# Performance work log

Measured on AMD Instinct MI355X. Metric: run time of the kernel, lower is better.

Reference implementation:

```python
import jax, jax.numpy as jnp
import numpy as np

N = 30000        # nodes
E = 480000       # edges (before self-loops)
F_IN = 512       # input feature dim
HID = 64         # per-head hidden dim
HEADS = 4
WIDTH = HID * HEADS  # 256, concat heads
LAYERS = 3
NCLS = 40
NEG_SLOPE = 0.2


def setup_inputs() -> dict:
    key = jax.random.key(0)
    ks = jax.random.split(key, 16)
    def p(k, shape, scale=0.1):
        return jax.random.normal(k, shape, dtype=jnp.float32) * scale
    return {
        "x": jax.random.normal(ks[0], (N, F_IN), dtype=jnp.float32),
        "edge_index": jax.random.randint(ks[1], (2, E), 0, N, dtype=jnp.int32),
        # layer 1: F_IN -> HEADS*HID (concat)
        "W1": p(ks[2], (F_IN, WIDTH)), "as1": p(ks[3], (HEADS, HID)), "ad1": p(ks[4], (HEADS, HID)), "b1": p(ks[5], (WIDTH,)),
        # layer 2: WIDTH -> WIDTH
        "W2": p(ks[6], (WIDTH, WIDTH)), "as2": p(ks[7], (HEADS, HID)), "ad2": p(ks[8], (HEADS, HID)), "b2": p(ks[9], (WIDTH,)),
        # layer 3: WIDTH -> WIDTH
        "W3": p(ks[10], (WIDTH, WIDTH)), "as3": p(ks[11], (HEADS, HID)), "ad3": p(ks[12], (HEADS, HID)), "b3": p(ks[13], (WIDTH,)),
        # JK='cat' output head: WIDTH*LAYERS -> NCLS
        "Wo": p(ks[14], (WIDTH * LAYERS, NCLS)), "bo": p(ks[15], (NCLS,)),
    }


def gat_layer(x, Wm, a_src, a_dst, b, src, dst):
    # PyG GATConv (concat=True, eval mode): h = xW reshaped [N,H,C];
    # e_ij = leaky_relu(a_src.h_j + a_dst.h_i) for edge j->i, softmax over dst groups.
    n = x.shape[0]
    H, C = a_src.shape
    h = (x @ Wm).reshape(n, H, C)                      # [N,H,C]
    es = jnp.sum(h * a_src, axis=-1)                   # [N,H]
    ed = jnp.sum(h * a_dst, axis=-1)                   # [N,H]
    e = jax.nn.leaky_relu(es[src] + ed[dst], NEG_SLOPE)  # [Etot,H]
    m = jax.ops.segment_max(e, dst, num_segments=n)    # stable softmax per dst node
    w = jnp.exp(e - m[dst])
    den = jax.ops.segment_sum(w, dst, num_segments=n)
    alpha = w / den[dst]                               # [Etot,H]
    out = jax.ops.segment_sum(h[src] * alpha[:, :, None], dst, num_segments=n)  # [N,H,C]
    return out.reshape(n, H * C) + b


def reference(x, edge_index, W1, as1, ad1, b1, W2, as2, ad2, b2, W3, as3, ad3, b3, Wo, bo):
    # add self-loops (PyG GATConv default)
    loops = jnp.arange(N, dtype=edge_index.dtype)
    src = jnp.concatenate([edge_index[0], loops])
    dst = jnp.concatenate([edge_index[1], loops])
    # dropout is identity in eval mode
    h1 = jax.nn.relu(gat_layer(x, W1, as1, ad1, b1, src, dst))
    h2 = jax.nn.relu(gat_layer(h1, W2, as2, ad2, b2, src, dst))
    h3 = jax.nn.relu(gat_layer(h2, W3, as3, ad3, b3, src, dst))
    h = jnp.concatenate([h1, h2, h3], axis=-1)         # JK 'cat': [N, WIDTH*LAYERS]
    return h @ Wo + bo                                 # [N, NCLS]
```

## Files before the change

### kernel.cpp

```cpp
#include <hip/hip_runtime.h>

#define N_NODES 30000
#define N_EDGES 480000
#define ETOT    510000
#define F_IN    512
#define WIDTH   256
#define NCLS    40
#define KCAT    768
#define NPAD    48

typedef __attribute__((ext_vector_type(8))) short short8;
typedef __attribute__((ext_vector_type(4))) float f32x4;

__device__ __forceinline__ unsigned short f2bf(float f){
  unsigned u = __float_as_uint(f);
  u += 0x7fffu + ((u >> 16) & 1u);
  return (unsigned short)(u >> 16);
}
__device__ __forceinline__ float b2f(unsigned short s){
  return __uint_as_float(((unsigned)s) << 16);
}

__global__ void transpose_w_kernel(const float* __restrict__ W, unsigned short* __restrict__ Wt,
                                   int K, int Nc){
  int k = blockIdx.x * blockDim.x + threadIdx.x;
  int n = blockIdx.y;
  if (k < K) Wt[(size_t)n * K + k] = f2bf(W[(size_t)k * Nc + n]);
}

__global__ void transpose_wo_kernel(const float* __restrict__ Wo, unsigned short* __restrict__ WoT){
  int i = blockIdx.x * blockDim.x + threadIdx.x;
  if (i < NPAD * KCAT){
    int c = i / KCAT, k = i - c * KCAT;
    WoT[i] = (c < NCLS) ? f2bf(Wo[(size_t)k * NCLS + c]) : (unsigned short)0;
  }
}

__global__ void zero_kernel(int* __restrict__ p, int n){
  int i = blockIdx.x * blockDim.x + threadIdx.x;
  if (i < n) p[i] = 0;
}

__global__ void hist_kernel(const int* __restrict__ ei, int* __restrict__ counts){
  int e = blockIdx.x * blockDim.x + threadIdx.x;
  if (e < ETOT){
    int d = (e < N_EDGES) ? ei[N_EDGES + e] : (e - N_EDGES);
    atomicAdd(&counts[d], 1);
  }
}

__global__ __launch_bounds__(1024) void scan_kernel(const int* __restrict__ counts,
                                                    int* __restrict__ offsets,
                                                    int* __restrict__ cursor, int n){
  __shared__ int wsum[16];
  int tid = threadIdx.x, lane = tid & 63, wid = tid >> 6;
  int running = 0;
  int nchunks = (n + 1023) >> 10;
  for (int ch = 0; ch < nchunks; ++ch){
    int i = (ch << 10) + tid;
    int v = (i < n) ? counts[i] : 0;
    int x = v;
    #pragma unroll
    for (int off = 1; off < 64; off <<= 1){
      int t = __shfl_up(x, off, 64);
      if (lane >= off) x += t;
    }
    if (lane == 63) wsum[wid] = x;
    __syncthreads();
    if (wid == 0){
      int s = (lane < 16) ? wsum[lane] : 0;
      #pragma unroll
      for (int off = 1; off < 16; off <<= 1){
        int t = __shfl_up(s, off, 64);
        if (lane >= off) s += t;
      }
      if (lane < 16) wsum[lane] = s;
    }
    __syncthreads();
    int waveprefix = (wid > 0) ? wsum[wid - 1] : 0;
    int excl = x - v + waveprefix + running;
    if (i < n){ offsets[i] = excl; cursor[i] = excl; }
    running += wsum[15];
    __syncthreads();
  }
  if (tid == 0) offsets[n] = running;
}

__global__ void scatter_kernel(const int* __restrict__ ei, int* __restrict__ cursor,
                               int* __restrict__ srcs){
  int e = blockIdx.x * blockDim.x + threadIdx.x;
  if (e < ETOT){
    int s, d;
    if (e < N_EDGES){ s = ei[e]; d = ei[N_EDGES + e]; }
    else { s = e - N_EDGES; d = s; }
    int pos = atomicAdd(&cursor[d], 1);
    srcs[pos] = s;
  }
}

template<int K, bool AF32>
__global__ __launch_bounds__(256) void gemm_direct_kernel(const void* __restrict__ Araw,
                                                          const unsigned short* __restrict__ Bt,
                                                          const float* __restrict__ a_s,
                                                          const float* __restrict__ a_d,
                                                          float* __restrict__ es,
                                                          float* __restrict__ ed,
                                                          unsigned short* __restrict__ hb,
                                                          int M){
  int tid = threadIdx.x, lane = tid & 63, wid = tid >> 6;
  int l15 = lane & 15, quad = lane >> 4;
  int g = wid;
  int m0 = blockIdx.x * 64;

  int arow[4];
  #pragma unroll
  for (int rt = 0; rt < 4; ++rt){
    int r = m0 + rt * 16 + l15;
    arow[rt] = (r < M) ? r : (M - 1);
  }
  const unsigned short* brow[4];
  #pragma unroll
  for (int ct = 0; ct < 4; ++ct)
    brow[ct] = Bt + (size_t)(64 * g + ct * 16 + l15) * K + quad * 8;

  f32x4 acc[4][4];
  #pragma unroll
  for (int rt = 0; rt < 4; ++rt)
    #pragma unroll
    for (int ct = 0; ct < 4; ++ct) acc[rt][ct] = (f32x4){0.f, 0.f, 0.f, 0.f};

  auto load_a = [&](int rt, int k0) -> short8 {
    if (AF32){
      const float* p = (const float*)Araw + (size_t)arow[rt] * K + k0 + quad * 8;
      float4 v0 = *(const float4*)(p);
      float4 v1 = *(const float4*)(p + 4);
      union { short8 s; ushort4 u[2]; } r;
      r.u[0] = (ushort4){f2bf(v0.x), f2bf(v0.y), f2bf(v0.z), f2bf(v0.w)};
      r.u[1] = (ushort4){f2bf(v1.x), f2bf(v1.y), f2bf(v1.z), f2bf(v1.w)};
      return r.s;
    } else {
      return *(const short8*)((const unsigned short*)Araw + (size_t)arow[rt] * K + k0 + quad * 8);
    }
  };

  short8 a_cur[4], b_cur[4], a_nxt[4], b_nxt[4];
  #pragma unroll
  for (int rt = 0; rt < 4; ++rt) a_cur[rt] = load_a(rt, 0);
  #pragma unroll
  for (int ct = 0; ct < 4; ++ct) b_cur[ct] = *(const short8*)(brow[ct]);

  for (int k0 = 0; k0 < K; k0 += 32){
    if (k0 + 32 < K){
      #pragma unroll
      for (int rt = 0; rt < 4; ++rt) a_nxt[rt] = load_a(rt, k0 + 32);
      #pragma unroll
      for (int ct = 0; ct < 4; ++ct) b_nxt[ct] = *(const short8*)(brow[ct] + k0 + 32);
    }
    #pragma unroll
    for (int rt = 0; rt < 4; ++rt)
      #pragma unroll
      for (int ct = 0; ct < 4; ++ct)
        acc[rt][ct] = __builtin_amdgcn_mfma_f32_16x16x32_bf16(a_cur[rt], b_cur[ct], acc[rt][ct], 0, 0, 0);
    #pragma unroll
    for (int rt = 0; rt < 4; ++rt) a_cur[rt] = a_nxt[rt];
    #pragma unroll
    for (int ct = 0; ct < 4; ++ct) b_cur[ct] = b_nxt[ct];
  }

  #pragma unroll
  for (int rt = 0; rt < 4; ++rt){
    int row0 = m0 + rt * 16 + quad * 4;
    #pragma unroll
    for (int i = 0; i < 4; ++i){
      int grow = row0 + i;
      unsigned vo[4];
      #pragma unroll
      for (int ct = 0; ct < 4; ++ct){
        unsigned lo = (unsigned)f2bf(acc[rt][ct][i]);
        unsigned hi = (unsigned)__shfl_xor((int)lo, 1, 64);
        vo[ct] = lo | (hi << 16);
      }
      if ((l15 & 1) == 0 && grow < M){
        unsigned short* hrow = hb + (size_t)grow * WIDTH + 64 * g + l15;
        *(unsigned*)(hrow)      = vo[0];
        *(unsigned*)(hrow + 16) = vo[1];
        *(unsigned*)(hrow + 32) = vo[2];
        *(unsigned*)(hrow + 48) = vo[3];
      }
    }
  }

  float asv[4], adv[4];
  #pragma unroll
  for (int ct = 0; ct < 4; ++ct){
    asv[ct] = a_s[g * 64 + ct * 16 + l15];
    adv[ct] = a_d[g * 64 + ct * 16 + l15];
  }
  #pragma unroll
  for (int rt = 0; rt < 4; ++rt){
    int row0 = m0 + rt * 16 + quad * 4;
    #pragma unroll
    for (int i = 0; i < 4; ++i){
      float se = acc[rt][0][i] * asv[0] + acc[rt][1][i] * asv[1]
               + acc[rt][2][i] * asv[2] + acc[rt][3][i] * asv[3];
      float sd = acc[rt][0][i] * adv[0] + acc[rt][1][i] * adv[1]
               + acc[rt][2][i] * adv[2] + acc[rt][3][i] * adv[3];
      #pragma unroll
      for (int off = 1; off < 16; off <<= 1){
        se += __shfl_xor(se, off, 64);
        sd += __shfl_xor(sd, off, 64);
      }
      int grow = row0 + i;
      if (l15 == 0 && grow < M){
        es[grow * 4 + g] = se;
        ed[grow * 4 + g] = sd;
      }
    }
  }
}

__global__ __launch_bounds__(256) void agg_kernel(const int* __restrict__ offsets,
                                                  const int* __restrict__ srcs,
                                                  const float* __restrict__ es,
                                                  const float* __restrict__ ed,
                                                  const unsigned short* __restrict__ hb,
                                                  const float* __restrict__ bias,
                                                  unsigned short* __restrict__ hout){
  __shared__ float eLds[8][64][4];
  __shared__ int   sLds[8][64];
  int wid = threadIdx.x >> 6;
  int lane = threadIdx.x & 63;
  int half = lane >> 5, l32 = lane & 31;
  int slot = wid * 2 + half;
  int n = blockIdx.x * 8 + slot;
  int base = offsets[n];
  int deg = offsets[n + 1] - base;
  float4 edv = *(const float4*)(ed + n * 4);

  float m0 = -1e30f, m1 = -1e30f, m2 = -1e30f, m3 = -1e30f;
  for (int i = l32; i < deg; i += 32){
    int s = srcs[base + i];
    float4 ev = *(const float4*)(es + s * 4);
    float e0 = ev.x + edv.x, e1 = ev.y + edv.y, e2 = ev.z + edv.z, e3 = ev.w + edv.w;
    e0 = e0 > 0.f ? e0 : 0.2f * e0;
    e1 = e1 > 0.f ? e1 : 0.2f * e1;
    e2 = e2 > 0.f ? e2 : 0.2f * e2;
    e3 = e3 > 0.f ? e3 : 0.2f * e3;
    if (i < 64){
      sLds[slot][i] = s;
      *(float4*)(&eLds[slot][i][0]) = (float4){e0, e1, e2, e3};
    }
    m0 = fmaxf(m0, e0); m1 = fmaxf(m1, e1); m2 = fmaxf(m2, e2); m3 = fmaxf(m3, e3);
  }
  #pragma unroll
  for (int off = 1; off < 32; off <<= 1){
    m0 = fmaxf(m0, __shfl_xor(m0, off, 64));
    m1 = fmaxf(m1, __shfl_xor(m1, off, 64));
    m2 = fmaxf(m2, __shfl_xor(m2, off, 64));
    m3 = fmaxf(m3, __shfl_xor(m3, off, 64));
  }
  int head = l32 >> 3;
  float mh  = (head == 0) ? m0 : (head == 1) ? m1 : (head == 2) ? m2 : m3;
  float edh = (head == 0) ? edv.x : (head == 1) ? edv.y : (head == 2) ? edv.z : edv.w;

  float2 a0 = {0.f,0.f}, a1 = {0.f,0.f}, a2 = {0.f,0.f}, a3 = {0.f,0.f};
  float den = 0.f;
  const unsigned short* hcol = hb + 8 * l32;
  for (int i = 0; i < deg; i += 8){
    int sidx[8]; float w[8];
    #pragma unroll
    for (int u = 0; u < 8; ++u){
      int idx = i + u;
      bool v = idx < deg;
      float le; int s;
      if (idx < 64 || !v){
        int ic = v ? idx : 0;
        if (ic >= 64) ic = 0;
        s  = sLds[slot][ic];
        le = eLds[slot][ic][head];
      } else {
        s = srcs[base + idx];
        float e = es[s * 4 + head] + edh;
        le = e > 0.f ? e : 0.2f * e;
      }
      sidx[u] = s;
      w[u] = v ? __expf(le - mh) : 0.f;
    }
    uint4 hv[8];
    #pragma unroll
    for (int u = 0; u < 8; ++u)
      hv[u] = *(const uint4*)(hcol + (size_t)sidx[u] * WIDTH);
    #pragma unroll
    for (int u = 0; u < 8; ++u){
      float wu = w[u];
      den += wu;
      a0.x += wu * __uint_as_float(hv[u].x << 16);
      a0.y += wu * __uint_as_float(hv[u].x & 0xffff0000u);
      a1.x += wu * __uint_as_float(hv[u].y << 16);
      a1.y += wu * __uint_as_float(hv[u].y & 0xffff0000u);
      a2.x += wu * __uint_as_float(hv[u].z << 16);
      a2.y += wu * __uint_as_float(hv[u].z & 0xffff0000u);
      a3.x += wu * __uint_as_float(hv[u].w << 16);
      a3.y += wu * __uint_as_float(hv[u].w & 0xffff0000u);
    }
  }
  float inv = 1.0f / den;
  const float* bp = bias + 8 * l32;
  float4 bv0 = *(const float4*)(bp);
  float4 bv1 = *(const float4*)(bp + 4);
  float o0 = fmaxf(a0.x * inv + bv0.x, 0.f);
  float o1 = fmaxf(a0.y * inv + bv0.y, 0.f);
  float o2 = fmaxf(a1.x * inv + bv0.z, 0.f);
  float o3 = fmaxf(a1.y * inv + bv0.w, 0.f);
  float o4 = fmaxf(a2.x * inv + bv1.x, 0.f);
  float o5 = fmaxf(a2.y * inv + bv1.y, 0.f);
  float o6 = fmaxf(a3.x * inv + bv1.z, 0.f);
  float o7 = fmaxf(a3.y * inv + bv1.w, 0.f);
  uint4 o;
  o.x = (unsigned)f2bf(o0) | ((unsigned)f2bf(o1) << 16);
  o.y = (unsigned)f2bf(o2) | ((unsigned)f2bf(o3) << 16);
  o.z = (unsigned)f2bf(o4) | ((unsigned)f2bf(o5) << 16);
  o.w = (unsigned)f2bf(o6) | ((unsigned)f2bf(o7) << 16);
  *(uint4*)(hout + (size_t)n * WIDTH + 8 * l32) = o;
}

__global__ __launch_bounds__(256) void out_gemm_kernel(const unsigned short* __restrict__ h1,
                                                       const unsigned short* __restrict__ h2,
                                                       const unsigned short* __restrict__ h3,
                                                       const unsigned short* __restrict__ WoT,
                                                       const float* __restrict__ bo,
                                                       float* __restrict__ out){
  int tid = threadIdx.x, lane = tid & 63, wid = tid >> 6;
  int l15 = lane & 15, quad = lane >> 4;
  int m0 = blockIdx.x * 64 + 16 * wid;

  f32x4 acc[3];
  #pragma unroll
  for (int t = 0; t < 3; ++t) acc[t] = (f32x4){0.f, 0.f, 0.f, 0.f};

  int arow = m0 + l15; if (arow >= N_NODES) arow = N_NODES - 1;

  #pragma unroll
  for (int part = 0; part < 3; ++part){
    const unsigned short* hp = (part == 0) ? h1 : (part == 1) ? h2 : h3;
    const unsigned short* ap = hp + (size_t)arow * WIDTH;
    #pragma unroll
    for (int k0 = 0; k0 < WIDTH; k0 += 32){
      short8 af = *(const short8*)(ap + k0 + quad * 8);
      int kk = part * WIDTH + k0;
      #pragma unroll
      for (int t = 0; t < 3; ++t){
        short8 bf = *(const short8*)(WoT + (size_t)(16 * t + l15) * KCAT + kk + quad * 8);
        acc[t] = __builtin_amdgcn_mfma_f32_16x16x32_bf16(af, bf, acc[t], 0, 0, 0);
      }
    }
  }

  int r0 = m0 + quad * 4;
  #pragma unroll
  for (int t = 0; t < 3; ++t){
    int col = 16 * t + l15;
    if (col < NCLS){
      float bc = bo[col];
      #pragma unroll
      for (int r = 0; r < 4; ++r){
        int grow = r0 + r;
        if (grow < N_NODES) out[(size_t)grow * NCLS + col] = acc[t][r] + bc;
      }
    }
  }
}

static inline size_t align256(size_t x){ return (x + 255) & ~(size_t)255; }

extern "C" void kernel_launch(void* const* d_in, const int* in_sizes, int n_in,
                              void* d_out, int out_size, void* d_ws, size_t ws_size,
                              hipStream_t stream) {
  const float* x   = (const float*)d_in[0];
  const int*   ei  = (const int*)  d_in[1];
  const float* W1  = (const float*)d_in[2];
  const float* as1 = (const float*)d_in[3];
  const float* ad1 = (const float*)d_in[4];
  const float* b1  = (const float*)d_in[5];
  const float* W2  = (const float*)d_in[6];
  const float* as2 = (const float*)d_in[7];
  const float* ad2 = (const float*)d_in[8];
  const float* b2  = (const float*)d_in[9];
  const float* W3  = (const float*)d_in[10];
  const float* as3 = (const float*)d_in[11];
  const float* ad3 = (const float*)d_in[12];
  const float* b3  = (const float*)d_in[13];
  const float* Wo  = (const float*)d_in[14];
  const float* bo  = (const float*)d_in[15];
  float* out = (float*)d_out;

  char* p = (char*)d_ws;
  auto take = [&](size_t bytes) -> char* { char* cur = p; p += align256(bytes); return cur; };

  unsigned short* Wt1   = (unsigned short*)take((size_t)WIDTH * F_IN * 2);
  unsigned short* Wt2   = (unsigned short*)take((size_t)WIDTH * WIDTH * 2);
  unsigned short* Wt3   = (unsigned short*)take((size_t)WIDTH * WIDTH * 2);
  unsigned short* WoT   = (unsigned short*)take((size_t)NPAD * KCAT * 2);
  unsigned short* hstage= (unsigned short*)take((size_t)N_NODES * WIDTH * 2);
  float*          es    = (float*)take((size_t)N_NODES * 4 * 4);
  float*          ed    = (float*)take((size_t)N_NODES * 4 * 4);
  unsigned short* h1b   = (unsigned short*)take((size_t)N_NODES * WIDTH * 2);
  unsigned short* h2b   = (unsigned short*)take((size_t)N_NODES * WIDTH * 2);
  unsigned short* h3b   = (unsigned short*)take((size_t)N_NODES * WIDTH * 2);
  int*            counts  = (int*)take((size_t)N_NODES * 4);
  int*            offsets = (int*)take((size_t)(N_NODES + 1) * 4);
  int*            cursor  = (int*)take((size_t)N_NODES * 4);
  int*            srcs    = (int*)take((size_t)ETOT * 4);

  transpose_w_kernel<<<dim3(F_IN / 256, WIDTH), 256, 0, stream>>>(W1, Wt1, F_IN, WIDTH);
  transpose_w_kernel<<<dim3(1, WIDTH), 256, 0, stream>>>(W2, Wt2, WIDTH, WIDTH);
  transpose_w_kernel<<<dim3(1, WIDTH), 256, 0, stream>>>(W3, Wt3, WIDTH, WIDTH);
  transpose_wo_kernel<<<(NPAD * KCAT + 255) / 256, 256, 0, stream>>>(Wo, WoT);

  zero_kernel<<<(N_NODES + 255) / 256, 256, 0, stream>>>(counts, N_NODES);
  hist_kernel<<<(ETOT + 255) / 256, 256, 0, stream>>>(ei, counts);
  scan_kernel<<<1, 1024, 0, stream>>>(counts, offsets, cursor, N_NODES);
  scatter_kernel<<<(ETOT + 255) / 256, 256, 0, stream>>>(ei, cursor, srcs);

  const int ntiles   = (N_NODES + 63) / 64;
  const int agg_grid = N_NODES / 8;

  gemm_direct_kernel<F_IN, true><<<ntiles, 256, 0, stream>>>(x, Wt1, as1, ad1, es, ed, hstage, N_NODES);
  agg_kernel<<<agg_grid, 256, 0, stream>>>(offsets, srcs, es, ed, hstage, b1, h1b);
  gemm_direct_kernel<WIDTH, false><<<ntiles, 256, 0, stream>>>(h1b, Wt2, as2, ad2, es, ed, hstage, N_NODES);
  agg_kernel<<<agg_grid, 256, 0, stream>>>(offsets, srcs, es, ed, hstage, b2, h2b);
  gemm_direct_kernel<WIDTH, false><<<ntiles, 256, 0, stream>>>(h2b, Wt3, as3, ad3, es, ed, hstage, N_NODES);
  agg_kernel<<<agg_grid, 256, 0, stream>>>(offsets, srcs, es, ed, hstage, b3, h3b);

  out_gemm_kernel<<<ntiles, 256, 0, stream>>>(h1b, h2b, h3b, WoT, bo, out);
}
```

Baseline: 435.9 us.

## Stage GEMM operands in LDS via global_load_lds and pre-cast x to bf16

Replaces the register-direct GEMM, where each wave loaded its own A and B fragments from global memory, with a kernel that stages a 64x32 A tile and a 256x32 B tile in LDS using async global-to-LDS loads. All four waves then share them. A separate cast kernel converts x to bf16 up front, so the first-layer GEMM reads half the bytes and does no conversion inline. The trade-off is an extra full pass over x plus a 30 MB workspace buffer. The new loop also has two barriers per K step and no software prefetch or double buffering, so load latency is no longer hidden.

```diff
diff --git a/kernel.cpp b/kernel.cpp
--- a/kernel.cpp
+++ b/kernel.cpp
@@ -19,6 +19,25 @@
 }
 __device__ __forceinline__ float b2f(unsigned short s){
   return __uint_as_float(((unsigned)s) << 16);
+}
+
+__device__ __forceinline__ void load_lds16(const void* g, void* l){
+  __builtin_amdgcn_global_load_lds((const __attribute__((address_space(1))) void*)g,
+                                   (__attribute__((address_space(3))) void*)l, 16, 0, 0);
+}
+
+__global__ void cast8_kernel(const float* __restrict__ in, unsigned short* __restrict__ out, int n8){
+  int i = blockIdx.x * blockDim.x + threadIdx.x;
+  if (i < n8){
+    const float4* p = (const float4*)(in + 8 * (size_t)i);
+    float4 v0 = p[0], v1 = p[1];
+    uint4 o;
+    o.x = (unsigned)f2bf(v0.x) | ((unsigned)f2bf(v0.y) << 16);
+    o.y = (unsigned)f2bf(v0.z) | ((unsigned)f2bf(v0.w) << 16);
+    o.z = (unsigned)f2bf(v1.x) | ((unsigned)f2bf(v1.y) << 16);
+    o.w = (unsigned)f2bf(v1.z) | ((unsigned)f2bf(v1.w) << 16);
+    *(uint4*)(out + 8 * (size_t)i) = o;
+  }
 }
 
 __global__ void transpose_w_kernel(const float* __restrict__ W, unsigned short* __restrict__ Wt,
@@ -98,74 +117,54 @@
   }
 }
 
-template<int K, bool AF32>
-__global__ __launch_bounds__(256) void gemm_direct_kernel(const void* __restrict__ Araw,
-                                                          const unsigned short* __restrict__ Bt,
-                                                          const float* __restrict__ a_s,
-                                                          const float* __restrict__ a_d,
-                                                          float* __restrict__ es,
-                                                          float* __restrict__ ed,
-                                                          unsigned short* __restrict__ hb,
-                                                          int M){
+template<int K>
+__global__ __launch_bounds__(256) void gemm_lds_kernel(const unsigned short* __restrict__ A,
+                                                       const unsigned short* __restrict__ Bt,
+                                                       const float* __restrict__ a_s,
+                                                       const float* __restrict__ a_d,
+                                                       float* __restrict__ es,
+                                                       float* __restrict__ ed,
+                                                       unsigned short* __restrict__ hb,
+                                                       int M){
+  __shared__ unsigned short Als[64 * 32];
+  __shared__ unsigned short Bls[256 * 32];
   int tid = threadIdx.x, lane = tid & 63, wid = tid >> 6;
   int l15 = lane & 15, quad = lane >> 4;
+  int m0 = blockIdx.x * 64;
+
+  int srow = m0 + lane; if (srow >= M) srow = M - 1;
+  const unsigned short* aptr = A + (size_t)srow * K + wid * 8;
+  const unsigned short* bptr = Bt + (size_t)tid * K;
+
+  f32x4 acc[4][4];
+  #pragma unroll
+  for (int rt = 0; rt < 4; ++rt)
+    #pragma unroll
+    for (int ct = 0; ct < 4; ++ct) acc[rt][ct] = (f32x4){0.f, 0.f, 0.f, 0.f};
+
+  for (int k0 = 0; k0 < K; k0 += 32){
+    __syncthreads();
+    load_lds16(aptr + k0,      &Als[tid * 8]);
+    load_lds16(bptr + k0,      &Bls[(0 * 256 + tid) * 8]);
+    load_lds16(bptr + k0 + 8,  &Bls[(1 * 256 + tid) * 8]);
+    load_lds16(bptr + k0 + 16, &Bls[(2 * 256 + tid) * 8]);
+    load_lds16(bptr + k0 + 24, &Bls[(3 * 256 + tid) * 8]);
+    __syncthreads();
+    short8 af[4], bf[4];
+    #pragma unroll
+    for (int rt = 0; rt < 4; ++rt)
+      af[rt] = *(const short8*)(&Als[(quad * 64 + rt * 16 + l15) * 8]);
+    #pragma unroll
+    for (int ct = 0; ct < 4; ++ct)
+      bf[ct] = *(const short8*)(&Bls[(quad * 256 + wid * 64 + ct * 16 + l15) * 8]);
+    #pragma unroll
+    for (int rt = 0; rt < 4; ++rt)
+      #pragma unroll
+      for (int ct = 0; ct < 4; ++ct)
+        acc[rt][ct] = __builtin_amdgcn_mfma_f32_16x16x32_bf16(af[rt], bf[ct], acc[rt][ct], 0, 0, 0);
+  }
+
   int g = wid;
-  int m0 = blockIdx.x * 64;
-
-  int arow[4];
-  #pragma unroll
-  for (int rt = 0; rt < 4; ++rt){
-    int r = m0 + rt * 16 + l15;
-    arow[rt] = (r < M) ? r : (M - 1);
-  }
-  const unsigned short* brow[4];
-  #pragma unroll
-  for (int ct = 0; ct < 4; ++ct)
-    brow[ct] = Bt + (size_t)(64 * g + ct * 16 + l15) * K + quad * 8;
-
-  f32x4 acc[4][4];
-  #pragma unroll
-  for (int rt = 0; rt < 4; ++rt)
-    #pragma unroll
-    for (int ct = 0; ct < 4; ++ct) acc[rt][ct] = (f32x4){0.f, 0.f, 0.f, 0.f};
-
-  auto load_a = [&](int rt, int k0) -> short8 {
-    if (AF32){
-      const float* p = (const float*)Araw + (size_t)arow[rt] * K + k0 + quad * 8;
-      float4 v0 = *(const float4*)(p);
-      float4 v1 = *(const float4*)(p + 4);
-      union { short8 s; ushort4 u[2]; } r;
-      r.u[0] = (ushort4){f2bf(v0.x), f2bf(v0.y), f2bf(v0.z), f2bf(v0.w)};
-      r.u[1] = (ushort4){f2bf(v1.x), f2bf(v1.y), f2bf(v1.z), f2bf(v1.w)};
-      return r.s;
-    } else {
-      return *(const short8*)((const unsigned short*)Araw + (size_t)arow[rt] * K + k0 + quad * 8);
-    }
-  };
-
-  short8 a_cur[4], b_cur[4], a_nxt[4], b_nxt[4];
-  #pragma unroll
-  for (int rt = 0; rt < 4; ++rt) a_cur[rt] = load_a(rt, 0);
-  #pragma unroll
-  for (int ct = 0; ct < 4; ++ct) b_cur[ct] = *(const short8*)(brow[ct]);
-
-  for (int k0 = 0; k0 < K; k0 += 32){
-    if (k0 + 32 < K){
-      #pragma unroll
-      for (int rt = 0; rt < 4; ++rt) a_nxt[rt] = load_a(rt, k0 + 32);
-      #pragma unroll
-      for (int ct = 0; ct < 4; ++ct) b_nxt[ct] = *(const short8*)(brow[ct] + k0 + 32);
-    }
-    #pragma unroll
-    for (int rt = 0; rt < 4; ++rt)
-      #pragma unroll
-      for (int ct = 0; ct < 4; ++ct)
-        acc[rt][ct] = __builtin_amdgcn_mfma_f32_16x16x32_bf16(a_cur[rt], b_cur[ct], acc[rt][ct], 0, 0, 0);
-    #pragma unroll
-    for (int rt = 0; rt < 4; ++rt) a_cur[rt] = a_nxt[rt];
-    #pragma unroll
-    for (int ct = 0; ct < 4; ++ct) b_cur[ct] = b_nxt[ct];
-  }
 
   #pragma unroll
   for (int rt = 0; rt < 4; ++rt){
@@ -397,6 +396,7 @@
   char* p = (char*)d_ws;
   auto take = [&](size_t bytes) -> char* { char* cur = p; p += align256(bytes); return cur; };
 
+  unsigned short* xb    = (unsigned short*)take((size_t)N_NODES * F_IN * 2);
   unsigned short* Wt1   = (unsigned short*)take((size_t)WIDTH * F_IN * 2);
   unsigned short* Wt2   = (unsigned short*)take((size_t)WIDTH * WIDTH * 2);
   unsigned short* Wt3   = (unsigned short*)take((size_t)WIDTH * WIDTH * 2);
@@ -412,6 +412,7 @@
   int*            cursor  = (int*)take((size_t)N_NODES * 4);
   int*            srcs    = (int*)take((size_t)ETOT * 4);
 
+  cast8_kernel<<<(N_NODES * F_IN / 8 + 255) / 256, 256, 0, stream>>>(x, xb, N_NODES * F_IN / 8);
   transpose_w_kernel<<<dim3(F_IN / 256, WIDTH), 256, 0, stream>>>(W1, Wt1, F_IN, WIDTH);
   transpose_w_kernel<<<dim3(1, WIDTH), 256, 0, stream>>>(W2, Wt2, WIDTH, WIDTH);
   transpose_w_kernel<<<dim3(1, WIDTH), 256, 0, stream>>>(W3, Wt3, WIDTH, WIDTH);
@@ -425,11 +426,11 @@
   const int ntiles   = (N_NODES + 63) / 64;
   const int agg_grid = N_NODES / 8;
 
-  gemm_direct_kernel<F_IN, true><<<ntiles, 256, 0, stream>>>(x, Wt1, as1, ad1, es, ed, hstage, N_NODES);
+  gemm_lds_kernel<F_IN><<<ntiles, 256, 0, stream>>>(xb, Wt1, as1, ad1, es, ed, hstage, N_NODES);
   agg_kernel<<<agg_grid, 256, 0, stream>>>(offsets, srcs, es, ed, hstage, b1, h1b);
-  gemm_direct_kernel<WIDTH, false><<<ntiles, 256, 0, stream>>>(h1b, Wt2, as2, ad2, es, ed, hstage, N_NODES);
+  gemm_lds_kernel<WIDTH><<<ntiles, 256, 0, stream>>>(h1b, Wt2, as2, ad2, es, ed, hstage, N_NODES);
   agg_kernel<<<agg_grid, 256, 0, stream>>>(offsets, srcs, es, ed, hstage, b2, h2b);
-  gemm_direct_kernel<WIDTH, false><<<ntiles, 256, 0, stream>>>(h2b, Wt3, as3, ad3, es, ed, hstage, N_NODES);
+  gemm_lds_kernel<WIDTH><<<ntiles, 256, 0, stream>>>(h2b, Wt3, as3, ad3, es, ed, hstage, N_NODES);
   agg_kernel<<<agg_grid, 256, 0, stream>>>(offsets, srcs, es, ed, hstage, b3, h3b);
 
   out_gemm_kernel<<<ntiles, 256, 0, stream>>>(h1b, h2b, h3b, WoT, bo, out);
```

Measured after the change: 420.2 us. 1.04x faster.
